# Performance work log

Hardware: AMD Instinct MI355X
Metric: run time of the kernel (lower is better)

## Reference

```python
import jax, jax.numpy as jnp
import numpy as np

# ---- static config matching init_kwargs ----
LEVELS = np.array([8, 8, 8, 6, 5], dtype=np.int64)  # per-iteration FSQ levels
K = 4          # number of residual-quantization iterations (len(levels))
EPS = 1e-3
BIG = 1e8

_half_l = (LEVELS - 1) * (1.0 - EPS) / 2.0                     # bound half-width
_offset_b = np.where(LEVELS % 2 == 1, 0.0, 0.5)                # bound offset
_shift_b = np.tan(_offset_b / _half_l)                         # bound shift
_offset_q = np.where(LEVELS % 2 == 1, 0.0, 0.3)                # quantize offset
_states = np.round(np.stack([-_half_l, _half_l], 0) - _offset_q)  # (2, d) valid step range per dim
_steps = np.arange(_states.min(), _states.max() + 1.0)         # (C,) global integer grid
_mask = (_states[0][:, None] <= _steps[None, :]) & (_steps[None, :] <= _states[1][:, None])  # (d, C)
_half_width = (LEVELS // 2).astype(np.float64)
C = _steps.shape[0]  # = 8 for these levels
D = LEVELS.shape[0]  # = 5


def _round_ste_soft(z, temp, g):
    """Soft rounding with straight-through gradients. z: (N, d), temp: (1,), g: (N, d, C) gumbel."""
    steps = jnp.asarray(_steps, z.dtype)
    mask = jnp.asarray(_mask)
    d2 = (z[..., None] - steps) ** 2                      # (N, d, C) squared distances
    d2 = jnp.where(mask, d2, jnp.asarray(BIG, z.dtype))   # mask out-of-range steps (matches d*mask + 1e8*~mask)
    alpha = 1.0 / temp
    d2 = (alpha - 1.0) * jax.lax.stop_gradient(d2) + d2   # temperature trick on detached distances
    logits = -d2 / temp
    A = jax.nn.softmax(logits, axis=-1)
    # gumbel-max sampling == torch.multinomial over A (same categorical distribution)
    code = jnp.argmax(jax.lax.stop_gradient(logits) + g, axis=-1)  # (N, d) int
    oh = jax.nn.one_hot(code, C, dtype=A.dtype)
    # A2 forward value == one_hot(code); gradient flows through A
    A2 = A + jax.lax.stop_gradient(oh * (1.0 - A) - (1.0 - oh) * A)
    return z + A2 @ steps - jax.lax.stop_gradient(z)       # STE: value = hard code, grad = identity


def _quantize(h, temp_eff, g):
    half_l = jnp.asarray(_half_l, h.dtype)
    shift = jnp.asarray(_shift_b, h.dtype)
    offset = jnp.asarray(_offset_b, h.dtype)
    z = jnp.tanh(h + shift) * half_l - offset              # bound()
    q = _round_ste_soft(z, temp_eff, g)
    return q / jnp.asarray(_half_width, h.dtype)


def setup_inputs() -> dict:
    key = jax.random.key(0)
    ks = jax.random.split(key, 7)
    N, E = 65536, 1024
    h_in = jax.random.normal(ks[0], (N, E), jnp.float32)
    W_proj = jax.random.normal(ks[1], (K, D, E), jnp.float32) / np.sqrt(E).astype(np.float32)
    b_proj = jax.random.normal(ks[2], (K, D), jnp.float32) * 0.01
    W_inv = jax.random.normal(ks[3], (K, E, D), jnp.float32) / np.sqrt(D).astype(np.float32)
    b_inv = jax.random.normal(ks[4], (K, E), jnp.float32) * 0.01
    temp = jnp.ones((1,), jnp.float32)
    u = jax.random.uniform(ks[5], (K, N, D, C), jnp.float32)   # uniform noise for categorical sampling
    p = jax.random.uniform(ks[6], (N,), jnp.float32)            # torch.rand(h_in.shape[0])
    return {"h_in": h_in, "W_proj": W_proj, "b_proj": b_proj, "W_inv": W_inv,
            "b_inv": b_inv, "temp": temp, "u": u, "p": p}


def reference(h_in, W_proj, b_proj, W_inv, b_inv, temp, u, p):
    g = -jnp.log(-jnp.log(u + 1e-20) + 1e-20)               # gumbel noise from uniforms
    temp_eff = jnp.maximum(temp ** 2, 1e-8)                  # (1,)
    r = h_in
    q = jnp.zeros_like(h_in)
    q_mix = jnp.zeros_like(h_in)
    codes = []
    for i in range(K):  # loop over structurally distinct RVQ stages
        h_i = r @ W_proj[i].T + b_proj[i]                    # (N, d)
        z_i = _quantize(h_i, temp_eff, g[i])                 # (N, d)
        q_i = z_i @ W_inv[i].T + b_inv[i]                    # (N, E)
        r = r - q_i
        q = q + q_i
        codes.append(z_i)
        sel = ((i / K) < p) & (p <= ((i + 1) / K))           # (N,) bool
        q_mix = q_mix + q * sel[:, None].astype(q.dtype)
    vq_code = jnp.concatenate(codes, axis=-1)                # (N, K*d)
    vq_loss = jnp.mean(jnp.linalg.norm(h_in - q_mix, axis=-1))
    return q, vq_code, vq_loss
```

## Files before the change

kernel.cpp:

```cpp
#include <hip/hip_runtime.h>
#include <cmath>

#define NROWS 65536
#define EDIM  1024
#define KST   4

__global__ __launch_bounds__(256) void winv_transpose(const float* __restrict__ W_inv,
                                                      float* __restrict__ WiT) {
    const int t = blockIdx.x * 256 + threadIdx.x;
    const int i = t >> 10;
    const int e = t & 1023;
    const float* src = W_inv + (size_t)i * 5120 + (size_t)e * 5;
    const float w0 = src[0], w1 = src[1], w2 = src[2], w3 = src[3], w4 = src[4];
    float* dst = WiT + (size_t)i * 5120 + e;
    dst[0]    = w0;
    dst[1024] = w1;
    dst[2048] = w2;
    dst[3072] = w3;
    dst[4096] = w4;
}

__global__ __launch_bounds__(256, 2) void rvq_fused(
    const float* __restrict__ h_in,
    const float* __restrict__ W_proj,
    const float* __restrict__ b_proj,
    const float* __restrict__ WiT,
    const float* __restrict__ b_inv,
    const float* __restrict__ temp,
    const float* __restrict__ u,
    const float* __restrict__ p,
    float* __restrict__ out_q,
    float* __restrict__ out_code,
    float* __restrict__ out_loss,
    float shift012, float shift3)
{
    __shared__ float sW[11264];
    __shared__ float sLoss[4];

    const int tid  = threadIdx.x;
    const int lane = tid & 63;
    const int wib  = tid >> 6;
    const int wid  = blockIdx.x * 4 + wib;
    const int row0 = wid * 2;

    int dl = lane >> 3; if (dl > 4) dl = 4;
    const int   cl     = lane & 7;
    const float stepf  = (float)(cl - 4);
    const bool  valid  = (dl < 3) || (dl == 3 && cl >= 1 && cl <= 6)
                                  || (dl == 4 && cl >= 2 && cl <= 6);
    const float shiftd = (dl < 3) ? shift012 : ((dl == 3) ? shift3 : 0.0f);
    const float halfld = (dl < 3) ? 3.4965f : ((dl == 3) ? 2.4975f : 1.998f);
    const float offd   = (dl == 4) ? 0.0f : 0.5f;
    const float invhwd = (dl < 3) ? 0.25f : ((dl == 3) ? (1.0f/3.0f) : 0.5f);
    const int   ulane  = (lane < 40) ? lane : 39;

    const float tval = temp[0];
    const float te = fmaxf(tval * tval, 1e-8f);
    const float inv_te  = 1.0f / te;
    const float alpham1 = inv_te - 1.0f;

    float uu[KST][2];
    #pragma unroll
    for (int i = 0; i < KST; ++i)
        #pragma unroll
        for (int rr = 0; rr < 2; ++rr)
            uu[i][rr] = u[(size_t)i * 2621440 + (size_t)(row0 + rr) * 40 + ulane];

    float4 r4[2][4];
    float  p_r[2];
    float  ss[2];
    #pragma unroll
    for (int rr = 0; rr < 2; ++rr) {
        const float4* src = (const float4*)(h_in + (size_t)(row0 + rr) * EDIM);
        #pragma unroll
        for (int j = 0; j < 4; ++j) r4[rr][j] = src[lane + 64 * j];
        p_r[rr] = p[row0 + rr];
        float s = 0.f;
        #pragma unroll
        for (int j = 0; j < 4; ++j) {
            s = fmaf(r4[rr][j].x, r4[rr][j].x, s);
            s = fmaf(r4[rr][j].y, r4[rr][j].y, s);
            s = fmaf(r4[rr][j].z, r4[rr][j].z, s);
            s = fmaf(r4[rr][j].w, r4[rr][j].w, s);
        }
        ss[rr] = (p_r[rr] <= 0.0f) ? s : 0.0f;
    }

    for (int i = 0; i < KST; ++i) {
        __syncthreads();
        {
            const float4* gp = (const float4*)(W_proj + (size_t)i * 5120);
            float4* sp = (float4*)sW;
            #pragma unroll
            for (int k = 0; k < 5; ++k) sp[tid + k * 256] = gp[tid + k * 256];
            const float4* gw = (const float4*)(WiT + (size_t)i * 5120);
            float4* sw2 = (float4*)(sW + 5120);
            #pragma unroll
            for (int k = 0; k < 5; ++k) sw2[tid + k * 256] = gw[tid + k * 256];
            ((float4*)(sW + 10240))[tid] =
                ((const float4*)(b_inv + (size_t)i * EDIM))[tid];
        }
        __syncthreads();

        float hd[5][2];
        #pragma unroll
        for (int d = 0; d < 5; ++d) {
            const float bp = b_proj[i * 5 + d];
            float a0 = 0.f, a1 = 0.f;
            #pragma unroll
            for (int j = 0; j < 4; ++j) {
                const float4 w = *(const float4*)&sW[d * 1024 + 4 * lane + 256 * j];
                a0 = fmaf(w.x, r4[0][j].x, a0); a0 = fmaf(w.y, r4[0][j].y, a0);
                a0 = fmaf(w.z, r4[0][j].z, a0); a0 = fmaf(w.w, r4[0][j].w, a0);
                a1 = fmaf(w.x, r4[1][j].x, a1); a1 = fmaf(w.y, r4[1][j].y, a1);
                a1 = fmaf(w.z, r4[1][j].z, a1); a1 = fmaf(w.w, r4[1][j].w, a1);
            }
            float av[2] = {a0, a1};
            #pragma unroll
            for (int rr = 0; rr < 2; ++rr) {
                float v = av[rr];
                v += __shfl_xor(v, 1);
                v += __shfl_xor(v, 2);
                v += __shfl_xor(v, 4);
                v += __shfl_xor(v, 8);
                v += __shfl_xor(v, 16);
                v += __shfl_xor(v, 32);
                hd[d][rr] = v + bp;
            }
        }

        float zq_mine[2];
        #pragma unroll
        for (int rr = 0; rr < 2; ++rr) {
            float hsel = hd[0][rr];
            hsel = (dl == 1) ? hd[1][rr] : hsel;
            hsel = (dl == 2) ? hd[2][rr] : hsel;
            hsel = (dl == 3) ? hd[3][rr] : hsel;
            hsel = (dl == 4) ? hd[4][rr] : hsel;
            const float z  = __fsub_rn(__fmul_rn(tanhf(hsel + shiftd), halfld), offd);
            const float g1 = logf(uu[i][rr] + 1e-20f);
            const float g  = -logf(-g1 + 1e-20f);
            const float df = __fsub_rn(z, stepf);
            float d2 = __fmul_rn(df, df);
            d2 = valid ? d2 : 1e8f;
            const float d2x = fmaf(alpham1, d2, d2);
            float y   = -(d2x * inv_te) + g;
            int   idx = cl;
            #pragma unroll
            for (int m = 1; m <= 4; m <<= 1) {
                const float yo = __shfl_xor(y, m);
                const int   io = __shfl_xor(idx, m);
                const bool take = (yo > y) || (yo == y && io < idx);
                y   = take ? yo : y;
                idx = take ? io : idx;
            }
            zq_mine[rr] = (float)(idx - 4) * invhwd;
        }
        if (lane < 40 && cl == 0) {
            #pragma unroll
            for (int rr = 0; rr < 2; ++rr)
                out_code[(size_t)(row0 + rr) * 20 + i * 5 + dl] = zq_mine[rr];
        }

        float zq[5][2];
        #pragma unroll
        for (int d = 0; d < 5; ++d)
            #pragma unroll
            for (int rr = 0; rr < 2; ++rr)
                zq[d][rr] = __int_as_float(
                    __builtin_amdgcn_readlane(__float_as_int(zq_mine[rr]), d * 8));

        #pragma unroll
        for (int j = 0; j < 4; ++j) {
            const int eo = 4 * lane + 256 * j;
            const float4 b  = *(const float4*)&sW[10240 + eo];
            const float4 w0 = *(const float4*)&sW[5120 + eo];
            const float4 w1 = *(const float4*)&sW[6144 + eo];
            const float4 w2 = *(const float4*)&sW[7168 + eo];
            const float4 w3 = *(const float4*)&sW[8192 + eo];
            const float4 w4 = *(const float4*)&sW[9216 + eo];
            #pragma unroll
            for (int rr = 0; rr < 2; ++rr) {
                float tx = b.x, ty = b.y, tz = b.z, tw = b.w;
                tx = fmaf(zq[0][rr], w0.x, tx); ty = fmaf(zq[0][rr], w0.y, ty);
                tz = fmaf(zq[0][rr], w0.z, tz); tw = fmaf(zq[0][rr], w0.w, tw);
                tx = fmaf(zq[1][rr], w1.x, tx); ty = fmaf(zq[1][rr], w1.y, ty);
                tz = fmaf(zq[1][rr], w1.z, tz); tw = fmaf(zq[1][rr], w1.w, tw);
                tx = fmaf(zq[2][rr], w2.x, tx); ty = fmaf(zq[2][rr], w2.y, ty);
                tz = fmaf(zq[2][rr], w2.z, tz); tw = fmaf(zq[2][rr], w2.w, tw);
                tx = fmaf(zq[3][rr], w3.x, tx); ty = fmaf(zq[3][rr], w3.y, ty);
                tz = fmaf(zq[3][rr], w3.z, tz); tw = fmaf(zq[3][rr], w3.w, tw);
                tx = fmaf(zq[4][rr], w4.x, tx); ty = fmaf(zq[4][rr], w4.y, ty);
                tz = fmaf(zq[4][rr], w4.z, tz); tw = fmaf(zq[4][rr], w4.w, tw);
                r4[rr][j].x -= tx; r4[rr][j].y -= ty;
                r4[rr][j].z -= tz; r4[rr][j].w -= tw;
            }
        }

        const float lo = i * 0.25f, hi = (i + 1) * 0.25f;
        #pragma unroll
        for (int rr = 0; rr < 2; ++rr) {
            if (lo < p_r[rr] && p_r[rr] <= hi) {
                float s = 0.f;
                #pragma unroll
                for (int j = 0; j < 4; ++j) {
                    s = fmaf(r4[rr][j].x, r4[rr][j].x, s);
                    s = fmaf(r4[rr][j].y, r4[rr][j].y, s);
                    s = fmaf(r4[rr][j].z, r4[rr][j].z, s);
                    s = fmaf(r4[rr][j].w, r4[rr][j].w, s);
                }
                ss[rr] = s;
            }
        }
    }

    float lsum = 0.f;
    #pragma unroll
    for (int rr = 0; rr < 2; ++rr) {
        float v = ss[rr];
        v += __shfl_xor(v, 1);
        v += __shfl_xor(v, 2);
        v += __shfl_xor(v, 4);
        v += __shfl_xor(v, 8);
        v += __shfl_xor(v, 16);
        v += __shfl_xor(v, 32);
        lsum += sqrtf(v);
    }
    #pragma unroll
    for (int rr = 0; rr < 2; ++rr) {
        const float4* src = (const float4*)(h_in + (size_t)(row0 + rr) * EDIM);
        float4* dst = (float4*)(out_q + (size_t)(row0 + rr) * EDIM);
        #pragma unroll
        for (int j = 0; j < 4; ++j) {
            const float4 h = src[lane + 64 * j];
            float4 o;
            o.x = h.x - r4[rr][j].x;
            o.y = h.y - r4[rr][j].y;
            o.z = h.z - r4[rr][j].z;
            o.w = h.w - r4[rr][j].w;
            dst[lane + 64 * j] = o;
        }
    }
    if (lane == 0) sLoss[wib] = lsum;
    __syncthreads();
    if (tid == 0) {
        const float bl = (sLoss[0] + sLoss[1]) + (sLoss[2] + sLoss[3]);
        atomicAdd(out_loss, bl * (1.0f / 65536.0f));
    }
}

extern "C" void kernel_launch(void* const* d_in, const int* in_sizes, int n_in,
                              void* d_out, int out_size, void* d_ws, size_t ws_size,
                              hipStream_t stream) {
    (void)in_sizes; (void)n_in; (void)out_size; (void)ws_size;
    const float* h_in   = (const float*)d_in[0];
    const float* W_proj = (const float*)d_in[1];
    const float* b_proj = (const float*)d_in[2];
    const float* W_inv  = (const float*)d_in[3];
    const float* b_inv  = (const float*)d_in[4];
    const float* temp   = (const float*)d_in[5];
    const float* u      = (const float*)d_in[6];
    const float* p      = (const float*)d_in[7];

    float* out_q    = (float*)d_out;
    float* out_code = out_q + (size_t)NROWS * EDIM;
    float* out_loss = out_code + (size_t)NROWS * 20;

    float* WiT = (float*)d_ws;

    hipMemsetAsync(out_loss, 0, sizeof(float), stream);

    hipLaunchKernelGGL(winv_transpose, dim3(16), dim3(256), 0, stream, W_inv, WiT);

    double hl01 = (8.0 - 1.0) * (1.0 - 1e-3) / 2.0;
    double hl3  = (6.0 - 1.0) * (1.0 - 1e-3) / 2.0;
    float shift012 = (float)std::tan(0.5 / hl01);
    float shift3   = (float)std::tan(0.5 / hl3);

    dim3 grid(NROWS / 8);
    dim3 block(256);
    hipLaunchKernelGGL(rvq_fused, grid, block, 0, stream,
                       h_in, W_proj, b_proj, WiT, b_inv, temp, u, p,
                       out_q, out_code, out_loss, shift012, shift3);
}
```

Measured before the change: 676.6 us.

## Stream W_proj and b_inv from global, prefetch W_inv into registers before barrier

W_proj is now read directly from global (L2-cached) in the projection instead of being staged in LDS, and b_inv is loaded straight into registers. W_inv is loaded into registers before the first barrier and written to a smaller LDS buffer, with the second barrier moved to just before the inverse projection. The aim is to cut LDS footprint and the serialized staging stalls, overlapping the W_inv load with the projection and quantization work. In exchange each wave issues more global loads for W_proj and holds more registers, which may lower occupancy.

```diff
diff --git a/kernel.cpp b/kernel.cpp
--- a/kernel.cpp
+++ b/kernel.cpp
@@ -34,7 +34,7 @@
     float* __restrict__ out_loss,
     float shift012, float shift3)
 {
-    __shared__ float sW[11264];
+    __shared__ float sWi[5120];
     __shared__ float sLoss[4];
 
     const int tid  = threadIdx.x;
@@ -87,29 +87,31 @@
     }
 
     for (int i = 0; i < KST; ++i) {
+        const float4* gw = (const float4*)(WiT + (size_t)i * 5120);
+        float4 wreg[5];
+        #pragma unroll
+        for (int k = 0; k < 5; ++k) wreg[k] = gw[tid + k * 256];
+        const float4* bvp = (const float4*)(b_inv + (size_t)i * EDIM);
+        float4 bv[4];
+        #pragma unroll
+        for (int j = 0; j < 4; ++j) bv[j] = bvp[lane + 64 * j];
+
         __syncthreads();
         {
-            const float4* gp = (const float4*)(W_proj + (size_t)i * 5120);
-            float4* sp = (float4*)sW;
-            #pragma unroll
-            for (int k = 0; k < 5; ++k) sp[tid + k * 256] = gp[tid + k * 256];
-            const float4* gw = (const float4*)(WiT + (size_t)i * 5120);
-            float4* sw2 = (float4*)(sW + 5120);
-            #pragma unroll
-            for (int k = 0; k < 5; ++k) sw2[tid + k * 256] = gw[tid + k * 256];
-            ((float4*)(sW + 10240))[tid] =
-                ((const float4*)(b_inv + (size_t)i * EDIM))[tid];
-        }
-        __syncthreads();
+            float4* sw = (float4*)sWi;
+            #pragma unroll
+            for (int k = 0; k < 5; ++k) sw[tid + k * 256] = wreg[k];
+        }
 
         float hd[5][2];
         #pragma unroll
         for (int d = 0; d < 5; ++d) {
             const float bp = b_proj[i * 5 + d];
+            const float4* wp = (const float4*)(W_proj + (size_t)i * 5120 + (size_t)d * 1024);
             float a0 = 0.f, a1 = 0.f;
             #pragma unroll
             for (int j = 0; j < 4; ++j) {
-                const float4 w = *(const float4*)&sW[d * 1024 + 4 * lane + 256 * j];
+                const float4 w = wp[lane + 64 * j];
                 a0 = fmaf(w.x, r4[0][j].x, a0); a0 = fmaf(w.y, r4[0][j].y, a0);
                 a0 = fmaf(w.z, r4[0][j].z, a0); a0 = fmaf(w.w, r4[0][j].w, a0);
                 a1 = fmaf(w.x, r4[1][j].x, a1); a1 = fmaf(w.y, r4[1][j].y, a1);
@@ -170,15 +172,17 @@
                 zq[d][rr] = __int_as_float(
                     __builtin_amdgcn_readlane(__float_as_int(zq_mine[rr]), d * 8));
 
+        __syncthreads();
+
         #pragma unroll
         for (int j = 0; j < 4; ++j) {
             const int eo = 4 * lane + 256 * j;
-            const float4 b  = *(const float4*)&sW[10240 + eo];
-            const float4 w0 = *(const float4*)&sW[5120 + eo];
-            const float4 w1 = *(const float4*)&sW[6144 + eo];
-            const float4 w2 = *(const float4*)&sW[7168 + eo];
-            const float4 w3 = *(const float4*)&sW[8192 + eo];
-            const float4 w4 = *(const float4*)&sW[9216 + eo];
+            const float4 b  = bv[j];
+            const float4 w0 = *(const float4*)&sWi[eo];
+            const float4 w1 = *(const float4*)&sWi[1024 + eo];
+            const float4 w2 = *(const float4*)&sWi[2048 + eo];
+            const float4 w3 = *(const float4*)&sWi[3072 + eo];
+            const float4 w4 = *(const float4*)&sWi[4096 + eo];
             #pragma unroll
             for (int rr = 0; rr < 2; ++rr) {
                 float tx = b.x, ty = b.y, tz = b.z, tw = b.w;
```

New measurement: 817.5 us. 1.21x slower.
